# Performance work log

Hardware: AMD Instinct MI355X
Metric: run time of the kernel (lower is better)

The kernel has to match this reference:

```python
import jax, jax.numpy as jnp
import numpy as np

B, S, T = 64, 80, 20          # batch, video_len, caption_len
F, H, E, V, CD = 4096, 256, 256, 32000, 64  # feat, hidden, embed, vocab, coverage_dim
LN_EPS = 1e-5


def setup_inputs() -> dict:
    key = jax.random.key(0)
    ks = iter(jax.random.split(key, 40))
    rn = lambda *shape: jax.random.normal(next(ks), shape, dtype=jnp.float32) * 0.05
    inp = {
        "video_features": jax.random.normal(next(ks), (B, S, F), dtype=jnp.float32),
        "captions": jax.random.randint(next(ks), (B, T), 0, V),
        # video projection
        "W_vp": rn(H, F), "b_vp": jnp.zeros((H,), jnp.float32),
        # encoder LSTM (2 layers)
        "enc_Wih0": rn(4 * H, H), "enc_Whh0": rn(4 * H, H),
        "enc_bih0": jnp.zeros((4 * H,), jnp.float32), "enc_bhh0": jnp.zeros((4 * H,), jnp.float32),
        "enc_Wih1": rn(4 * H, H), "enc_Whh1": rn(4 * H, H),
        "enc_bih1": jnp.zeros((4 * H,), jnp.float32), "enc_bhh1": jnp.zeros((4 * H,), jnp.float32),
        # word embedding
        "emb": jax.random.uniform(next(ks), (V, E), jnp.float32, -0.1, 0.1),
        # decoder LSTM (input = E + H)
        "dec_Wih0": rn(4 * H, E + H), "dec_Whh0": rn(4 * H, H),
        "dec_bih0": jnp.zeros((4 * H,), jnp.float32), "dec_bhh0": jnp.zeros((4 * H,), jnp.float32),
        "dec_Wih1": rn(4 * H, H), "dec_Whh1": rn(4 * H, H),
        "dec_bih1": jnp.zeros((4 * H,), jnp.float32), "dec_bhh1": jnp.zeros((4 * H,), jnp.float32),
        # attention
        "att_Wh": rn(H, H), "att_Ws": rn(H, H),
        "att_v": jax.random.normal(next(ks), (H,), dtype=jnp.float32) * 0.1,
        "att_Wc": rn(H, CD),
        "cov_w": rn(CD, 1, 3), "cov_b": jnp.zeros((CD,), jnp.float32),
        # output layernorm + projection
        "ln_g": jnp.ones((H,), jnp.float32), "ln_b": jnp.zeros((H,), jnp.float32),
        "W_out": rn(V, H), "b_out": jnp.zeros((V,), jnp.float32),
    }
    return inp


def _lstm_cell(x, h, c, Wih, Whh, bih, bhh):
    z = x @ Wih.T + h @ Whh.T + bih + bhh
    i, f, g, o = jnp.split(z, 4, axis=-1)  # torch gate order: i, f, g, o
    c_new = jax.nn.sigmoid(f) * c + jax.nn.sigmoid(i) * jnp.tanh(g)
    h_new = jax.nn.sigmoid(o) * jnp.tanh(c_new)
    return h_new, c_new


def reference(video_features, captions, W_vp, b_vp,
              enc_Wih0, enc_Whh0, enc_bih0, enc_bhh0,
              enc_Wih1, enc_Whh1, enc_bih1, enc_bhh1,
              emb,
              dec_Wih0, dec_Whh0, dec_bih0, dec_bhh0,
              dec_Wih1, dec_Whh1, dec_bih1, dec_bhh1,
              att_Wh, att_Ws, att_v, att_Wc, cov_w, cov_b,
              ln_g, ln_b, W_out, b_out):
    b = video_features.shape[0]
    # ---- encoder ----
    vp = video_features @ W_vp.T + b_vp  # [B,S,H]

    def enc_step(carry, x_t):
        h1, c1, h2, c2 = carry
        h1, c1 = _lstm_cell(x_t, h1, c1, enc_Wih0, enc_Whh0, enc_bih0, enc_bhh0)
        h2, c2 = _lstm_cell(h1, h2, c2, enc_Wih1, enc_Whh1, enc_bih1, enc_bhh1)
        return (h1, c1, h2, c2), h2

    z = jnp.zeros((b, H), vp.dtype)
    (eh1, ec1, eh2, ec2), enc_out = jax.lax.scan(enc_step, (z, z, z, z), vp.transpose(1, 0, 2))
    enc_out = enc_out.transpose(1, 0, 2)  # [B,S,H]

    enc_proj = enc_out @ att_Wh.T  # [B,S,H], invariant over decode steps
    cov_k = cov_w[:, 0, :]          # [CD,3]

    def dec_step(carry, tok):
        h1, c1, h2, c2, cov = carry
        # attention with coverage (decoder_hidden[0][-1] == top-layer h)
        padded = jnp.pad(cov, ((0, 0), (1, 1)))
        win = jnp.stack([padded[:, :-2], padded[:, 1:-1], padded[:, 2:]], axis=-1)  # [B,S,3]
        cov_feat = jnp.einsum("bsk,ck->bsc", win, cov_k) + cov_b  # conv1d k=3 pad=1
        cov_proj = cov_feat @ att_Wc.T                              # [B,S,H]
        dec_proj = h2 @ att_Ws.T                                    # [B,H]
        energy = jnp.tanh(enc_proj + dec_proj[:, None, :] + cov_proj)
        scores = energy @ att_v                                     # [B,S]
        attn = jax.nn.softmax(scores, axis=1)
        ctx = jnp.einsum("bs,bsh->bh", attn, enc_out)
        new_cov = cov + attn
        # decoder LSTM step
        x = jnp.concatenate([emb[tok], ctx], axis=-1)  # [B,E+H]
        h1, c1 = _lstm_cell(x, h1, c1, dec_Wih0, dec_Whh0, dec_bih0, dec_bhh0)
        h2, c2 = _lstm_cell(h1, h2, c2, dec_Wih1, dec_Whh1, dec_bih1, dec_bhh1)
        # layernorm + vocab projection
        mu = jnp.mean(h2, axis=-1, keepdims=True)
        var = jnp.mean((h2 - mu) ** 2, axis=-1, keepdims=True)
        normed = (h2 - mu) * jax.lax.rsqrt(var + LN_EPS) * ln_g + ln_b
        logits = normed @ W_out.T + b_out  # [B,V]
        return (h1, c1, h2, c2, new_cov), logits

    cov0 = jnp.zeros((b, enc_out.shape[1]), enc_out.dtype)
    _, logits = jax.lax.scan(dec_step, (eh1, ec1, eh2, ec2, cov0), captions.T)
    return logits.transpose(1, 0, 2)  # [B,T,V]
```

## Files before the change

kernel.cpp:

```cpp
#include <hip/hip_runtime.h>
#include <math.h>

#define BB 64
#define SS 80
#define TT 20
#define FF 4096
#define HH 256
#define VV 32000

typedef __attribute__((ext_vector_type(8))) short bf16x8;
typedef __attribute__((ext_vector_type(4))) float f32x4;

__device__ __forceinline__ float fsig(float x){ return 1.f/(1.f+__expf(-x)); }
__device__ __forceinline__ float ftanh(float x){
    float xc = fminf(fmaxf(x,-15.f),15.f);
    float e = __expf(2.f*xc);
    return (e-1.f)/(e+1.f);
}
__device__ __forceinline__ unsigned int f2b(float x){
    unsigned int u = __float_as_uint(x);
    return (u + 0x7fffu + ((u>>16)&1u)) >> 16;
}
__device__ __forceinline__ float b2f(unsigned short u){
    return __uint_as_float(((unsigned)u)<<16);
}
__device__ __forceinline__ float dot2bf(unsigned w, unsigned hp, float acc){
    float r;
    asm("v_dot2_f32_bf16 %0, %1, %2, %3" : "=v"(r) : "v"(w), "v"(hp), "v"(acc));
    return r;
}
__device__ __forceinline__ void pack8(const float* __restrict__ s, unsigned short* __restrict__ d){
    float4 a = *reinterpret_cast<const float4*>(s);
    float4 b = *reinterpret_cast<const float4*>(s+4);
    uint4 o;
    o.x = f2b(a.x) | (f2b(a.y)<<16);
    o.y = f2b(a.z) | (f2b(a.w)<<16);
    o.z = f2b(b.x) | (f2b(b.y)<<16);
    o.w = f2b(b.z) | (f2b(b.w)<<16);
    *reinterpret_cast<uint4*>(d) = o;
}

__global__ __launch_bounds__(256) void prep_kernel(
    const float* __restrict__ eWhh0, const float* __restrict__ eWih1, const float* __restrict__ eWhh1,
    const float* __restrict__ dWih0, const float* __restrict__ dWhh0, const float* __restrict__ dWih1,
    const float* __restrict__ dWhh1, const float* __restrict__ attWs, const float* __restrict__ attWc,
    const float* __restrict__ cov_w, const float* __restrict__ cov_b,
    const float* __restrict__ e_bih0, const float* __restrict__ e_bhh0,
    const float* __restrict__ e_bih1, const float* __restrict__ e_bhh1,
    const float* __restrict__ d_bih0, const float* __restrict__ d_bhh0,
    const float* __restrict__ d_bih1, const float* __restrict__ d_bhh1,
    const float* __restrict__ W_out, const float* __restrict__ attWh,
    const float* __restrict__ W_vp,  const float* __restrict__ eWih0,
    const float* __restrict__ video, const float* __restrict__ emb,
    const int*   __restrict__ captions,
    unsigned* pkWhh0e, unsigned* pkWhh1e, unsigned* pkWih1e,
    unsigned* pkWx0d, unsigned* pkWhh0d, unsigned* pkWih1d, unsigned* pkWhh1d,
    unsigned* pkWs,
    float* M3, float* attcb,
    float* b0e, float* b1e, float* b0d, float* b1d,
    unsigned short* Wob, unsigned short* Whb,
    unsigned short* Wvpb, unsigned short* Wih0b, unsigned short* dWx0b,
    unsigned short* embg, unsigned short* vidb)
{
    int blk = blockIdx.x, tid = threadIdx.x;
    if (blk < 1856){
        const float* src; int stride, coff, Nj, j0, k0; unsigned* dst;
        if (blk < 1792){
            int mat = blk >> 8, tl = blk & 255;
            switch(mat){
                case 0: src=eWhh0; stride=256; coff=0;   dst=pkWhh0e; break;
                case 1: src=eWhh1; stride=256; coff=0;   dst=pkWhh1e; break;
                case 2: src=eWih1; stride=256; coff=0;   dst=pkWih1e; break;
                case 3: src=dWih0; stride=512; coff=256; dst=pkWx0d;  break;
                case 4: src=dWhh0; stride=256; coff=0;   dst=pkWhh0d; break;
                case 5: src=dWih1; stride=256; coff=0;   dst=pkWih1d; break;
                default:src=dWhh1; stride=256; coff=0;   dst=pkWhh1d; break;
            }
            Nj = 1024; j0 = (tl>>3)*32; k0 = (tl&7)*32;
        } else {
            int tl = blk - 1792;
            src=attWs; stride=256; coff=0; dst=pkWs;
            Nj = 256; j0 = (tl>>3)*32; k0 = (tl&7)*32;
        }
        __shared__ float t1[32][33];
        int r = tid >> 5, c = tid & 31;
        #pragma unroll
        for (int i=0;i<4;i++)
            t1[r+i*8][c] = src[(size_t)(j0+r+i*8)*stride + coff + k0 + c];
        __syncthreads();
        int k2l = tid >> 5, j = tid & 31;
        #pragma unroll
        for (int i=0;i<2;i++){
            int kq = k2l + i*8;
            dst[(size_t)(k0/2 + kq)*Nj + j0 + j] =
                f2b(t1[j][2*kq]) | (f2b(t1[j][2*kq+1])<<16);
        }
        return;
    }
    if (blk == 1856){
        float m0=0.f,m1=0.f,m2=0.f,cb=0.f;
        for (int c=0;c<64;c++){
            float w = attWc[tid*64+c];
            m0 += w*cov_w[c*3+0]; m1 += w*cov_w[c*3+1]; m2 += w*cov_w[c*3+2];
            cb += w*cov_b[c];
        }
        M3[tid*3+0]=m0; M3[tid*3+1]=m1; M3[tid*3+2]=m2; attcb[tid]=cb;
        return;
    }
    if (blk == 1857){
        for (int i=tid;i<1024;i+=256){
            b0e[i]=e_bih0[i]+e_bhh0[i]; b1e[i]=e_bih1[i]+e_bhh1[i];
            b0d[i]=d_bih0[i]+d_bhh0[i]; b1d[i]=d_bih1[i]+d_bhh1[i];
        }
        return;
    }
    if (blk >= 6818){ size_t i=(size_t)(blk-6818)*2048 + tid*8; pack8(video+i, vidb+i); return; }
    if (blk >= 6658){ size_t i=(size_t)(blk-6658)*2048 + tid*8;
        int row = (int)(i>>8), col = (int)(i&255);
        pack8(emb + (size_t)captions[row]*256 + col, embg+i); return; }
    if (blk >= 6530){ size_t i=(size_t)(blk-6530)*2048 + tid*8;
        int j = (int)(i>>8), k = (int)(i&255);
        pack8(dWih0 + (size_t)j*512 + k, dWx0b+i); return; }
    if (blk >= 6402){ size_t i=(size_t)(blk-6402)*2048 + tid*8; pack8(eWih0+i, Wih0b+i); return; }
    if (blk >= 5890){ size_t i=(size_t)(blk-5890)*2048 + tid*8; pack8(W_vp+i, Wvpb+i); return; }
    if (blk >= 5858){ size_t i=(size_t)(blk-5858)*2048 + tid*8; pack8(attWh+i, Whb+i); return; }
    { size_t i=(size_t)(blk-1858)*2048 + tid*8; pack8(W_out+i, Wob+i); }
}

template<bool OUTBF>
__global__ __launch_bounds__(256) void gemm_bf16(int K, int N,
    const short* __restrict__ A, const short* __restrict__ Bw,
    const float* __restrict__ bias, void* __restrict__ out)
{
    int w = threadIdx.x >> 6, lane = threadIdx.x & 63;
    int m0 = blockIdx.y*64 + w*16, n0 = blockIdx.x*64;
    int row = lane & 15, kg = lane >> 4;
    const short* arow = A + (size_t)(m0 + row)*K + kg*8;
    f32x4 acc[4] = {};
    for (int kk=0; kk<K; kk+=32){
        bf16x8 a = *reinterpret_cast<const bf16x8*>(arow + kk);
        #pragma unroll
        for (int f=0; f<4; ++f){
            bf16x8 bfr = *reinterpret_cast<const bf16x8*>(
                Bw + (size_t)(n0 + f*16 + row)*K + kk + kg*8);
            acc[f] = __builtin_amdgcn_mfma_f32_16x16x32_bf16(a, bfr, acc[f], 0, 0, 0);
        }
    }
    #pragma unroll
    for (int f=0; f<4; ++f){
        int n = n0 + f*16 + row;
        float bv = bias ? bias[n] : 0.f;
        #pragma unroll
        for (int r=0; r<4; ++r){
            int m = m0 + kg*4 + r;
            float v = acc[f][r] + bv;
            if (OUTBF) ((unsigned short*)out)[(size_t)m*N + n] = (unsigned short)f2b(v);
            else       ((float*)out)[(size_t)m*N + n] = v;
        }
    }
}

#define RES_DOTS(a0,a1,a2,a3)                                              \
    _Pragma("unroll")                                                      \
    for (int g=0; g<24; g++){                                              \
        uint4 hc = hp4[g];                                                 \
        a0=dot2bf(wv0[4*g+0],hc.x,a0); a1=dot2bf(wv1[4*g+0],hc.x,a1);      \
        a2=dot2bf(wv0[4*g+1],hc.y,a2); a3=dot2bf(wv1[4*g+1],hc.y,a3);      \
        a0=dot2bf(wv0[4*g+2],hc.z,a0); a1=dot2bf(wv1[4*g+2],hc.z,a1);      \
        a2=dot2bf(wv0[4*g+3],hc.w,a2); a3=dot2bf(wv1[4*g+3],hc.w,a3);      \
    }                                                                      \
    _Pragma("unroll")                                                      \
    for (int g=0; g<8; g++){                                               \
        uint4 hc = hp4[24+g];                                              \
        uint4 w0 = ws[j0][g ^ p0];                                         \
        uint4 w1 = ws[j1][g ^ p1];                                         \
        a0=dot2bf(w0.x,hc.x,a0); a1=dot2bf(w1.x,hc.x,a1);                  \
        a2=dot2bf(w0.y,hc.y,a2); a3=dot2bf(w1.y,hc.y,a3);                  \
        a0=dot2bf(w0.z,hc.z,a0); a1=dot2bf(w1.z,hc.z,a1);                  \
        a2=dot2bf(w0.w,hc.w,a2); a3=dot2bf(w1.w,hc.w,a3);                  \
    }

__global__ __launch_bounds__(512, 2) void enc_pipe(
    const float* __restrict__ zx0,
    const unsigned* __restrict__ pkWhh0, const unsigned* __restrict__ pkWih1,
    const unsigned* __restrict__ pkWhh1, const float* __restrict__ b1e,
    unsigned* __restrict__ h1pub,
    float* __restrict__ z1pub,
    unsigned short* __restrict__ h2seq,
    unsigned short* __restrict__ hfin, float* __restrict__ cfin,
    unsigned* __restrict__ flagA, unsigned* __restrict__ flagB)
{
    __shared__ uint4 ws[1024][8];
    __shared__ uint4 hp4[32];
    __shared__ float zsf[256], zso[256];
    __shared__ float zsx[1024];
    int gid = blockIdx.x, tid = threadIdx.x;
    int stage = gid >> 6, b = gid & 63;
    const unsigned* pk = (stage==0) ? pkWhh0 : ((stage==1) ? pkWih1 : pkWhh1);
    int j0 = tid, j1 = tid + 512;
    unsigned wv0[96], wv1[96];
    #pragma unroll
    for (int kk=0; kk<96; kk++){
        wv0[kk] = pk[(size_t)kk*1024 + j0];
        wv1[kk] = pk[(size_t)kk*1024 + j1];
    }
    unsigned* wsu = (unsigned*)ws;
    for (int i = tid; i < 32*1024; i += 512){
        int kk = i >> 10, j = i & 1023;
        wsu[j*32 + (((kk>>2) ^ (j&7))<<2) + (kk&3)] = pk[(size_t)(96+kk)*1024 + j];
    }
    int p0 = j0 & 7, p1 = j1 & 7;

    if (stage == 0){
        float c = 0.f;
        if (tid < 128) ((unsigned*)hp4)[tid] = 0;
        __syncthreads();
        for (int t=0; t<SS; ++t){
            size_t row = (size_t)b*SS + t;
            float zxv0=0.f, zxv1=0.f, zxv2=0.f, zxv3=0.f;
            if (tid < 256){
                const float* zr = zx0 + row*1024;
                zxv0=zr[tid]; zxv1=zr[tid+256]; zxv2=zr[tid+512]; zxv3=zr[tid+768];
            }
            float a0=0.f,a1=0.f,a2=0.f,a3=0.f;
            RES_DOTS(a0,a1,a2,a3)
            if (tid >= 256){ zsf[tid-256] = a0+a2; zso[tid-256] = a1+a3; }
            __syncthreads();
            if (tid < 256){
                float i_ = zxv0 + a0+a2;
                float f_ = zxv1 + zsf[tid];
                float g_ = zxv2 + a1+a3;
                float o_ = zxv3 + zso[tid];
                float cn = fsig(f_)*c + fsig(i_)*ftanh(g_);
                c = cn;
                ((unsigned short*)hp4)[tid] = (unsigned short)f2b(fsig(o_)*ftanh(cn));
            }
            __syncthreads();
            if (tid < 128)
                __hip_atomic_store(&h1pub[row*128 + tid], ((unsigned*)hp4)[tid],
                                   __ATOMIC_RELAXED, __HIP_MEMORY_SCOPE_AGENT);
            asm volatile("s_waitcnt vmcnt(0)" ::: "memory");
            __syncthreads();
            if (tid == 0)
                __hip_atomic_store(&flagA[b], (unsigned)(t+1),
                                   __ATOMIC_RELAXED, __HIP_MEMORY_SCOPE_AGENT);
        }
        if (tid < 256){
            hfin[b*512 + tid] = ((unsigned short*)hp4)[tid];
            cfin[b*512 + tid] = c;
        }
    } else if (stage == 1){
        float bj0 = b1e[j0], bj1 = b1e[j1];
        __syncthreads();
        for (int t=0; t<SS; ++t){
            size_t row = (size_t)b*SS + t;
            if (tid == 0){
                while (__hip_atomic_load(&flagA[b], __ATOMIC_RELAXED,
                                         __HIP_MEMORY_SCOPE_AGENT) < (unsigned)(t+1))
                    __builtin_amdgcn_s_sleep(2);
            }
            __syncthreads();
            if (tid < 128)
                ((unsigned*)hp4)[tid] = __hip_atomic_load(&h1pub[row*128 + tid],
                                          __ATOMIC_RELAXED, __HIP_MEMORY_SCOPE_AGENT);
            __syncthreads();
            float a0=0.f,a1=0.f,a2=0.f,a3=0.f;
            RES_DOTS(a0,a1,a2,a3)
            __hip_atomic_store(&z1pub[row*1024 + j0], a0+a2+bj0,
                               __ATOMIC_RELAXED, __HIP_MEMORY_SCOPE_AGENT);
            __hip_atomic_store(&z1pub[row*1024 + j1], a1+a3+bj1,
                               __ATOMIC_RELAXED, __HIP_MEMORY_SCOPE_AGENT);
            asm volatile("s_waitcnt vmcnt(0)" ::: "memory");
            __syncthreads();
            if (tid == 0)
                __hip_atomic_store(&flagB[b], (unsigned)(t+1),
                                   __ATOMIC_RELAXED, __HIP_MEMORY_SCOPE_AGENT);
        }
    } else {
        float c = 0.f;
        if (tid < 128) ((unsigned*)hp4)[tid] = 0;
        __syncthreads();
        for (int t=0; t<SS; ++t){
            size_t row = (size_t)b*SS + t;
            if (tid == 0){
                while (__hip_atomic_load(&flagB[b], __ATOMIC_RELAXED,
                                         __HIP_MEMORY_SCOPE_AGENT) < (unsigned)(t+1))
                    __builtin_amdgcn_s_sleep(2);
            }
            __syncthreads();
            zsx[j0] = __hip_atomic_load(&z1pub[row*1024 + j0],
                        __ATOMIC_RELAXED, __HIP_MEMORY_SCOPE_AGENT);
            zsx[j1] = __hip_atomic_load(&z1pub[row*1024 + j1],
                        __ATOMIC_RELAXED, __HIP_MEMORY_SCOPE_AGENT);
            float a0=0.f,a1=0.f,a2=0.f,a3=0.f;
            RES_DOTS(a0,a1,a2,a3)
            if (tid >= 256){ zsf[tid-256] = a0+a2; zso[tid-256] = a1+a3; }
            __syncthreads();
            if (tid < 256){
                float i_ = zsx[tid]     + a0+a2;
                float f_ = zsx[tid+256] + zsf[tid];
                float g_ = zsx[tid+512] + a1+a3;
                float o_ = zsx[tid+768] + zso[tid];
                float cn = fsig(f_)*c + fsig(i_)*ftanh(g_);
                c = cn;
                float hn = fsig(o_)*ftanh(cn);
                unsigned short hb = (unsigned short)f2b(hn);
                ((unsigned short*)hp4)[tid] = hb;
                h2seq[row*256 + tid] = hb;
            }
            __syncthreads();
        }
        if (tid < 256){
            hfin[b*512 + 256 + tid] = ((unsigned short*)hp4)[tid];
            cfin[b*512 + 256 + tid] = c;
        }
    }
}

template<int ITERS>
__device__ __forceinline__ void dot_phase(const unsigned* __restrict__ wbase,
    const unsigned* __restrict__ hu, int k2base, int jq, float* __restrict__ zrow)
{
    float a0=0.f,a1=0.f,a2=0.f,a3=0.f;
    const uint4* wp = (const uint4*)(wbase + (size_t)k2base*1024 + jq*4);
    #pragma unroll 8
    for (int kk=0; kk<ITERS; ++kk){
        uint4 w = wp[(size_t)kk*256];
        unsigned hp = hu[k2base+kk];
        a0=dot2bf(w.x,hp,a0); a1=dot2bf(w.y,hp,a1);
        a2=dot2bf(w.z,hp,a2); a3=dot2bf(w.w,hp,a3);
    }
    zrow[jq*4+0]=a0; zrow[jq*4+1]=a1; zrow[jq*4+2]=a2; zrow[jq*4+3]=a3;
}

__global__ __launch_bounds__(1024) void dec_scan(
    const float* __restrict__ embproj,
    const unsigned* __restrict__ wx0, const unsigned* __restrict__ whh0,
    const unsigned* __restrict__ wih1, const unsigned* __restrict__ whh1,
    const unsigned* __restrict__ pkWs,
    const float* __restrict__ b1d,
    const unsigned short* __restrict__ encp,
    const unsigned short* __restrict__ enco,
    const float* __restrict__ att_v, const float* __restrict__ M3,
    const float* __restrict__ attcb,
    const float* __restrict__ ln_g, const float* __restrict__ ln_b,
    const float* __restrict__ encfC, const unsigned short* __restrict__ encfH,
    unsigned short* __restrict__ normedb)
{
    int b = blockIdx.x, tid = threadIdx.x;
    __shared__ unsigned short encpL[SS*256];
    __shared__ unsigned short encoL[SS*256];
    __shared__ unsigned short h1b[256], h2b[256], ctxb[256];
    __shared__ float c1s[256], c2s[256];
    __shared__ float zb[4][1024];
    __shared__ float covs[82], scs[80], attns[80], dps[256];
    __shared__ float red[16];
    {
        const uint4* sp = (const uint4*)(encp + (size_t)b*SS*256);
        const uint4* so = (const uint4*)(enco + (size_t)b*SS*256);
        uint4* dp = (uint4*)encpL;
        uint4* dq = (uint4*)encoL;
        for (int i=tid; i<SS*256/8; i+=1024){ dp[i] = sp[i]; dq[i] = so[i]; }
    }
    int h = tid & 255;
    float bz0=0.f,bz1=0.f,bz2=0.f,bz3=0.f, gg=0.f, bb2=0.f;
    if (tid < 256){
        h1b[tid] = encfH[b*512 + tid];
        h2b[tid] = encfH[b*512 + 256 + tid];
        c1s[tid] = encfC[b*512 + tid];
        c2s[tid] = encfC[b*512 + 256 + tid];
        bz0=b1d[tid]; bz1=b1d[tid+256]; bz2=b1d[tid+512]; bz3=b1d[tid+768];
        gg=ln_g[tid]; bb2=ln_b[tid];
    }
    if (tid < 82) covs[tid] = 0.f;
    int wv = tid >> 6, lane = tid & 63;
    float va[4], m30[4], m31[4], m32[4];
    #pragma unroll
    for (int i=0;i<4;i++){
        int hh = lane + i*64;
        va[i]=att_v[hh]; m30[i]=M3[hh*3]; m31[i]=M3[hh*3+1]; m32[i]=M3[hh*3+2];
    }
    int q   = tid >> 8;
    int jq  = tid & 255;
    int m1  = tid >> 9;
    int ks1 = (tid >> 8) & 1;
    const unsigned* h1u = (const unsigned*)h1b;
    const unsigned* h2u = (const unsigned*)h2b;
    const unsigned* cxu = (const unsigned*)ctxb;
    __syncthreads();
    for (int t=0; t<TT; ++t){
        {
            float acc = 0.f;
            const unsigned* wp = pkWs + (size_t)(q*32)*256 + h;
            #pragma unroll 8
            for (int kk=0; kk<32; ++kk)
                acc = dot2bf(wp[(size_t)kk*256], h2u[q*32+kk], acc);
            zb[q][h] = acc;
        }
        __syncthreads();
        if (tid < 256) dps[tid] = attcb[tid] + zb[0][tid]+zb[1][tid]+zb[2][tid]+zb[3][tid];
        __syncthreads();
        for (int s = wv*5; s < wv*5+5; ++s){
            float c0=covs[s], c1v=covs[s+1], c2v=covs[s+2];
            float p = 0.f;
            #pragma unroll
            for (int i=0;i<4;i++){
                int hh = lane + i*64;
                float e = b2f(encpL[s*256+hh]) + dps[hh]
                        + m30[i]*c0 + m31[i]*c1v + m32[i]*c2v;
                p += va[i]*ftanh(e);
            }
            #pragma unroll
            for (int off=32;off;off>>=1) p += __shfl_down(p, off);
            if (lane == 0) scs[s] = p;
        }
        __syncthreads();
        if (tid < 64){
            float a = scs[tid];
            float bsc = (tid < 16) ? scs[tid+64] : -3.4e38f;
            float mx = fmaxf(a, bsc);
            #pragma unroll
            for (int off=32;off;off>>=1) mx = fmaxf(mx, __shfl_xor(mx, off));
            float ea = __expf(a - mx);
            float eb = (tid < 16) ? __expf(bsc - mx) : 0.f;
            float sum = ea + eb;
            #pragma unroll
            for (int off=32;off;off>>=1) sum += __shfl_xor(sum, off);
            float inv = 1.f/sum;
            attns[tid] = ea*inv;
            if (tid < 16) attns[tid+64] = eb*inv;
        }
        __syncthreads();
        if (tid < 80) covs[tid+1] += attns[tid];
        {
            float acc = 0.f;
            for (int s=q*20; s<q*20+20; ++s)
                acc += attns[s]*b2f(encoL[s*256 + h]);
            zb[q][h] = acc;
        }
        __syncthreads();
        if (tid < 256)
            ctxb[h] = (unsigned short)f2b(zb[0][h]+zb[1][h]+zb[2][h]+zb[3][h]);
        float ep0=0.f,ep1=0.f,ep2=0.f,ep3=0.f;
        if (tid < 256){
            const float* er = embproj + ((size_t)b*TT + t)*1024;
            ep0=er[h]; ep1=er[h+256]; ep2=er[h+512]; ep3=er[h+768];
        }
        __syncthreads();
        dot_phase<64>(m1 ? whh0 : wx0, m1 ? h1u : cxu, ks1*64, jq, &zb[m1*2+ks1][0]);
        __syncthreads();
        if (tid < 256){
            float i_ = ep0+zb[0][h]+zb[1][h]+zb[2][h]+zb[3][h];
            float f_ = ep1+zb[0][h+256]+zb[1][h+256]+zb[2][h+256]+zb[3][h+256];
            float g_ = ep2+zb[0][h+512]+zb[1][h+512]+zb[2][h+512]+zb[3][h+512];
            float o_ = ep3+zb[0][h+768]+zb[1][h+768]+zb[2][h+768]+zb[3][h+768];
            float cn = fsig(f_)*c1s[h] + fsig(i_)*ftanh(g_);
            c1s[h] = cn;
            h1b[h] = (unsigned short)f2b(fsig(o_)*ftanh(cn));
        }
        __syncthreads();
        dot_phase<64>(m1 ? whh1 : wih1, m1 ? h2u : h1u, ks1*64, jq, &zb[m1*2+ks1][0]);
        __syncthreads();
        float hn = 0.f;
        if (tid < 256){
            float i_ = bz0+zb[0][h]+zb[1][h]+zb[2][h]+zb[3][h];
            float f_ = bz1+zb[0][h+256]+zb[1][h+256]+zb[2][h+256]+zb[3][h+256];
            float g_ = bz2+zb[0][h+512]+zb[1][h+512]+zb[2][h+512]+zb[3][h+512];
            float o_ = bz3+zb[0][h+768]+zb[1][h+768]+zb[2][h+768]+zb[3][h+768];
            float cn = fsig(f_)*c2s[h] + fsig(i_)*ftanh(g_);
            c2s[h] = cn;
            hn = fsig(o_)*ftanh(cn);
            h2b[h] = (unsigned short)f2b(hn);
        }
        float s1 = hn;
        #pragma unroll
        for (int off=32;off;off>>=1) s1 += __shfl_xor(s1, off);
        if (lane == 0) red[wv] = s1;
        __syncthreads();
        float mean = (red[0]+red[1]+red[2]+red[3]) * (1.f/256.f);
        __syncthreads();
        float d = (tid < 256) ? (hn - mean) : 0.f;
        float s2 = d*d;
        #pragma unroll
        for (int off=32;off;off>>=1) s2 += __shfl_xor(s2, off);
        if (lane == 0) red[wv] = s2;
        __syncthreads();
        float var = (red[0]+red[1]+red[2]+red[3]) * (1.f/256.f);
        if (tid < 256)
            normedb[((size_t)b*TT + t)*256 + h] =
                (unsigned short)f2b(d*rsqrtf(var + 1e-5f)*gg + bb2);
        __syncthreads();
    }
}

__global__ __launch_bounds__(256) void logits_mfma(
    const short* __restrict__ A, const short* __restrict__ Bw,
    const float* __restrict__ bias, float* __restrict__ out)
{
    int w = threadIdx.x >> 6, lane = threadIdx.x & 63;
    int n0 = blockIdx.x*64 + w*16;
    int row = lane & 15, kg = lane >> 4;
    bf16x8 bfr[8];
    const short* brow = Bw + (size_t)(n0 + row)*256 + kg*8;
    #pragma unroll
    for (int kk=0;kk<8;kk++) bfr[kk] = *reinterpret_cast<const bf16x8*>(brow + kk*32);
    float bv = bias[n0 + row];
    for (int mt=0; mt<80; ++mt){
        int m0 = mt*16;
        const short* arow = A + (size_t)(m0 + row)*256 + kg*8;
        f32x4 acc = {};
        #pragma unroll
        for (int kk=0;kk<8;kk++){
            bf16x8 a = *reinterpret_cast<const bf16x8*>(arow + kk*32);
            acc = __builtin_amdgcn_mfma_f32_16x16x32_bf16(a, bfr[kk], acc, 0, 0, 0);
        }
        #pragma unroll
        for (int r=0;r<4;r++){
            int m = m0 + kg*4 + r;
            out[(size_t)m*VV + n0 + row] = acc[r] + bv;
        }
    }
}

extern "C" void kernel_launch(void* const* d_in, const int* in_sizes, int n_in,
                              void* d_out, int out_size, void* d_ws, size_t ws_size,
                              hipStream_t stream)
{
    const float* video  = (const float*)d_in[0];
    const int*   caps   = (const int*)  d_in[1];
    const float* W_vp   = (const float*)d_in[2];
    const float* b_vp   = (const float*)d_in[3];
    const float* eWih0  = (const float*)d_in[4];
    const float* eWhh0  = (const float*)d_in[5];
    const float* e_bih0 = (const float*)d_in[6];
    const float* e_bhh0 = (const float*)d_in[7];
    const float* eWih1  = (const float*)d_in[8];
    const float* eWhh1  = (const float*)d_in[9];
    const float* e_bih1 = (const float*)d_in[10];
    const float* e_bhh1 = (const float*)d_in[11];
    const float* emb    = (const float*)d_in[12];
    const float* dWih0  = (const float*)d_in[13];
    const float* dWhh0  = (const float*)d_in[14];
    const float* d_bih0 = (const float*)d_in[15];
    const float* d_bhh0 = (const float*)d_in[16];
    const float* dWih1  = (const float*)d_in[17];
    const float* dWhh1  = (const float*)d_in[18];
    const float* d_bih1 = (const float*)d_in[19];
    const float* d_bhh1 = (const float*)d_in[20];
    const float* attWh  = (const float*)d_in[21];
    const float* attWs  = (const float*)d_in[22];
    const float* att_v  = (const float*)d_in[23];
    const float* attWc  = (const float*)d_in[24];
    const float* cov_w  = (const float*)d_in[25];
    const float* cov_b  = (const float*)d_in[26];
    const float* ln_g   = (const float*)d_in[27];
    const float* ln_b   = (const float*)d_in[28];
    const float* W_out  = (const float*)d_in[29];
    const float* b_out  = (const float*)d_in[30];
    float* out = (float*)d_out;

    float* W = (float*)d_ws;
    size_t o = 0;
    auto alloc = [&](size_t n){ size_t r = o; o += ((n + 63)/64)*64; return r; };

    float* U = W + alloc((size_t)10485760);
    unsigned short* vidb = (unsigned short*)U;
    float* z1pub = U;
    float* zx0     = W + alloc((size_t)SS*BB*1024);
    float* embproj = W + alloc((size_t)TT*BB*1024);
    unsigned short* vp_b  = (unsigned short*)(W + alloc((size_t)SS*BB*HH/2));
    unsigned short* embg  = (unsigned short*)(W + alloc((size_t)TT*BB*HH/2));
    unsigned short* encpb = (unsigned short*)(W + alloc((size_t)BB*SS*HH/2));
    unsigned short* normedb = (unsigned short*)(W + alloc((size_t)BB*TT*HH/2));
    unsigned* h1pub = (unsigned*)(W + alloc((size_t)SS*BB*128));
    unsigned short* h2seq = (unsigned short*)(W + alloc((size_t)SS*BB*HH/2));
    float* encfC   = W + alloc(BB*512);
    unsigned short* encfH = (unsigned short*)(W + alloc(BB*256));
    unsigned* flags = (unsigned*)(W + alloc(128));
    unsigned* pkWhh0e = (unsigned*)(W + alloc(128*1024));
    unsigned* pkWhh1e = (unsigned*)(W + alloc(128*1024));
    unsigned* pkWih1e = (unsigned*)(W + alloc(128*1024));
    unsigned* pkWx0d  = (unsigned*)(W + alloc(128*1024));
    unsigned* pkWhh0d = (unsigned*)(W + alloc(128*1024));
    unsigned* pkWih1d = (unsigned*)(W + alloc(128*1024));
    unsigned* pkWhh1d = (unsigned*)(W + alloc(128*1024));
    unsigned* pkWs    = (unsigned*)(W + alloc(128*256));
    float* M3      = W + alloc(768);
    float* attcb   = W + alloc(256);
    float* b0e     = W + alloc(1024);
    float* b1e     = W + alloc(1024);
    float* b0d     = W + alloc(1024);
    float* b1d     = W + alloc(1024);
    unsigned short* Wob   = (unsigned short*)(W + alloc((size_t)VV*HH/2));
    unsigned short* Whb   = (unsigned short*)(W + alloc(256*HH/2));
    unsigned short* Wvpb  = (unsigned short*)(W + alloc((size_t)HH*FF/2));
    unsigned short* Wih0b = (unsigned short*)(W + alloc(1024*HH/2));
    unsigned short* dWx0b = (unsigned short*)(W + alloc(1024*HH/2));
    (void)ws_size; (void)n_in; (void)in_sizes; (void)out_size;

    hipMemsetAsync(flags, 0, 128*sizeof(unsigned), stream);

    prep_kernel<<<17058, 256, 0, stream>>>(
        eWhh0, eWih1, eWhh1, dWih0, dWhh0, dWih1, dWhh1, attWs, attWc,
        cov_w, cov_b, e_bih0, e_bhh0, e_bih1, e_bhh1, d_bih0, d_bhh0, d_bih1, d_bhh1,
        W_out, attWh, W_vp, eWih0, video, emb, caps,
        pkWhh0e, pkWhh1e, pkWih1e, pkWx0d, pkWhh0d, pkWih1d, pkWhh1d, pkWs,
        M3, attcb, b0e, b1e, b0d, b1d,
        Wob, Whb, Wvpb, Wih0b, dWx0b, embg, vidb);

    gemm_bf16<true><<<dim3(4, 80), 256, 0, stream>>>(
        FF, HH, (const short*)vidb, (const short*)Wvpb, b_vp, vp_b);

    gemm_bf16<false><<<dim3(16, 80), 256, 0, stream>>>(
        HH, 1024, (const short*)vp_b, (const short*)Wih0b, b0e, zx0);

    gemm_bf16<false><<<dim3(16, 20), 256, 0, stream>>>(
        HH, 1024, (const short*)embg, (const short*)dWx0b, b0d, embproj);

    enc_pipe<<<192, 512, 0, stream>>>(zx0, pkWhh0e, pkWih1e, pkWhh1e, b1e,
                                      h1pub, z1pub, h2seq, encfH, encfC,
                                      flags, flags + 64);

    gemm_bf16<true><<<dim3(4, 80), 256, 0, stream>>>(
        HH, HH, (const short*)h2seq, (const short*)Whb, nullptr, encpb);

    dec_scan<<<64, 1024, 0, stream>>>(embproj, pkWx0d, pkWhh0d, pkWih1d, pkWhh1d,
                                      pkWs, b1d, encpb, h2seq, att_v, M3, attcb,
                                      ln_g, ln_b, encfC, encfH, normedb);

    logits_mfma<<<VV/64, 256, 0, stream>>>(
        (const short*)normedb, (const short*)Wob, b_out, out);
}
```

Before: 1.100 ms.

## Split decoder scan into attention blocks and MFMA LSTM gate blocks with flag sync

Replaces the per-batch decoder scan kernel (64 blocks of 1024 threads, dot2 GEMVs) with a fused kernel of 72 blocks. 64 blocks do per-batch attention and layernorm. 8 extra blocks compute the decoder LSTM gates for the whole batch with bf16 MFMA, each block owning a slice of the hidden dimension. Context and hidden states pass between blocks through global buffers guarded by atomic flags and spin waits. The aim is to replace the latency-bound per-batch GEMVs with batched matrix-core work. The cost is cross-block synchronisation latency on every timestep, and all 72 blocks must be co-resident or the spin waits deadlock.

```diff
diff --git a/kernel.cpp b/kernel.cpp
--- a/kernel.cpp
+++ b/kernel.cpp
@@ -38,6 +38,19 @@
     o.z = f2b(b.x) | (f2b(b.y)<<16);
     o.w = f2b(b.z) | (f2b(b.w)<<16);
     *reinterpret_cast<uint4*>(d) = o;
+}
+__device__ __forceinline__ unsigned aload(const unsigned* p){
+    return __hip_atomic_load((unsigned*)p, __ATOMIC_RELAXED, __HIP_MEMORY_SCOPE_AGENT);
+}
+__device__ __forceinline__ void astore(unsigned* p, unsigned v){
+    __hip_atomic_store(p, v, __ATOMIC_RELAXED, __HIP_MEMORY_SCOPE_AGENT);
+}
+__device__ __forceinline__ void waitF(const unsigned* f, int mask, unsigned tgt, int lane){
+    for (;;){
+        unsigned v = aload(&f[lane & mask]);
+        if (__all(v >= tgt)) break;
+        __builtin_amdgcn_s_sleep(1);
+    }
 }
 
 __global__ __launch_bounds__(256) void prep_kernel(
@@ -53,40 +66,33 @@
     const float* __restrict__ W_vp,  const float* __restrict__ eWih0,
     const float* __restrict__ video, const float* __restrict__ emb,
     const int*   __restrict__ captions,
-    unsigned* pkWhh0e, unsigned* pkWhh1e, unsigned* pkWih1e,
-    unsigned* pkWx0d, unsigned* pkWhh0d, unsigned* pkWih1d, unsigned* pkWhh1d,
-    unsigned* pkWs,
+    unsigned* pkWhh0e, unsigned* pkWih1e, unsigned* pkWhh1e, unsigned* pkWs,
     float* M3, float* attcb,
     float* b0e, float* b1e, float* b0d, float* b1d,
     unsigned short* Wob, unsigned short* Whb,
     unsigned short* Wvpb, unsigned short* Wih0b, unsigned short* dWx0b,
-    unsigned short* embg, unsigned short* vidb)
+    unsigned short* embg,
+    unsigned short* Wx0p, unsigned short* Whh0p, unsigned short* Wih1p, unsigned short* Whh1p,
+    unsigned short* vidb)
 {
     int blk = blockIdx.x, tid = threadIdx.x;
-    if (blk < 1856){
-        const float* src; int stride, coff, Nj, j0, k0; unsigned* dst;
-        if (blk < 1792){
+    if (blk < 832){
+        const float* src; int Nj, j0, k0; unsigned* dst;
+        if (blk < 768){
             int mat = blk >> 8, tl = blk & 255;
-            switch(mat){
-                case 0: src=eWhh0; stride=256; coff=0;   dst=pkWhh0e; break;
-                case 1: src=eWhh1; stride=256; coff=0;   dst=pkWhh1e; break;
-                case 2: src=eWih1; stride=256; coff=0;   dst=pkWih1e; break;
-                case 3: src=dWih0; stride=512; coff=256; dst=pkWx0d;  break;
-                case 4: src=dWhh0; stride=256; coff=0;   dst=pkWhh0d; break;
-                case 5: src=dWih1; stride=256; coff=0;   dst=pkWih1d; break;
-                default:src=dWhh1; stride=256; coff=0;   dst=pkWhh1d; break;
-            }
+            src = (mat==0) ? eWhh0 : ((mat==1) ? eWih1 : eWhh1);
+            dst = (mat==0) ? pkWhh0e : ((mat==1) ? pkWih1e : pkWhh1e);
             Nj = 1024; j0 = (tl>>3)*32; k0 = (tl&7)*32;
         } else {
-            int tl = blk - 1792;
-            src=attWs; stride=256; coff=0; dst=pkWs;
+            int tl = blk - 768;
+            src=attWs; dst=pkWs;
             Nj = 256; j0 = (tl>>3)*32; k0 = (tl&7)*32;
         }
         __shared__ float t1[32][33];
         int r = tid >> 5, c = tid & 31;
         #pragma unroll
         for (int i=0;i<4;i++)
-            t1[r+i*8][c] = src[(size_t)(j0+r+i*8)*stride + coff + k0 + c];
+            t1[r+i*8][c] = src[(size_t)(j0+r+i*8)*256 + k0 + c];
         __syncthreads();
         int k2l = tid >> 5, j = tid & 31;
         #pragma unroll
@@ -97,7 +103,7 @@
         }
         return;
     }
-    if (blk == 1856){
+    if (blk == 832){
         float m0=0.f,m1=0.f,m2=0.f,cb=0.f;
         for (int c=0;c<64;c++){
             float w = attWc[tid*64+c];
@@ -107,24 +113,30 @@
         M3[tid*3+0]=m0; M3[tid*3+1]=m1; M3[tid*3+2]=m2; attcb[tid]=cb;
         return;
     }
-    if (blk == 1857){
+    if (blk == 833){
         for (int i=tid;i<1024;i+=256){
             b0e[i]=e_bih0[i]+e_bhh0[i]; b1e[i]=e_bih1[i]+e_bhh1[i];
             b0d[i]=d_bih0[i]+d_bhh0[i]; b1d[i]=d_bih1[i]+d_bhh1[i];
         }
         return;
     }
-    if (blk >= 6818){ size_t i=(size_t)(blk-6818)*2048 + tid*8; pack8(video+i, vidb+i); return; }
-    if (blk >= 6658){ size_t i=(size_t)(blk-6658)*2048 + tid*8;
+    if (blk >= 6306){ size_t i=(size_t)(blk-6306)*2048 + tid*8; pack8(video+i, vidb+i); return; }
+    if (blk >= 6178){ size_t i=(size_t)(blk-6178)*2048 + tid*8; pack8(dWhh1+i, Whh1p+i); return; }
+    if (blk >= 6050){ size_t i=(size_t)(blk-6050)*2048 + tid*8; pack8(dWih1+i, Wih1p+i); return; }
+    if (blk >= 5922){ size_t i=(size_t)(blk-5922)*2048 + tid*8; pack8(dWhh0+i, Whh0p+i); return; }
+    if (blk >= 5794){ size_t i=(size_t)(blk-5794)*2048 + tid*8;
+        int j = (int)(i>>8), k = (int)(i&255);
+        pack8(dWih0 + (size_t)j*512 + 256 + k, Wx0p+i); return; }
+    if (blk >= 5634){ size_t i=(size_t)(blk-5634)*2048 + tid*8;
         int row = (int)(i>>8), col = (int)(i&255);
         pack8(emb + (size_t)captions[row]*256 + col, embg+i); return; }
-    if (blk >= 6530){ size_t i=(size_t)(blk-6530)*2048 + tid*8;
+    if (blk >= 5506){ size_t i=(size_t)(blk-5506)*2048 + tid*8;
         int j = (int)(i>>8), k = (int)(i&255);
         pack8(dWih0 + (size_t)j*512 + k, dWx0b+i); return; }
-    if (blk >= 6402){ size_t i=(size_t)(blk-6402)*2048 + tid*8; pack8(eWih0+i, Wih0b+i); return; }
-    if (blk >= 5890){ size_t i=(size_t)(blk-5890)*2048 + tid*8; pack8(W_vp+i, Wvpb+i); return; }
-    if (blk >= 5858){ size_t i=(size_t)(blk-5858)*2048 + tid*8; pack8(attWh+i, Whb+i); return; }
-    { size_t i=(size_t)(blk-1858)*2048 + tid*8; pack8(W_out+i, Wob+i); }
+    if (blk >= 5378){ size_t i=(size_t)(blk-5378)*2048 + tid*8; pack8(eWih0+i, Wih0b+i); return; }
+    if (blk >= 4866){ size_t i=(size_t)(blk-4866)*2048 + tid*8; pack8(W_vp+i, Wvpb+i); return; }
+    if (blk >= 4834){ size_t i=(size_t)(blk-4834)*2048 + tid*8; pack8(attWh+i, Whb+i); return; }
+    { size_t i=(size_t)(blk-834)*2048 + tid*8; pack8(W_out+i, Wob+i); }
 }
 
 template<bool OUTBF>
@@ -184,8 +196,7 @@
     const float* __restrict__ zx0,
     const unsigned* __restrict__ pkWhh0, const unsigned* __restrict__ pkWih1,
     const unsigned* __restrict__ pkWhh1, const float* __restrict__ b1e,
-    unsigned* __restrict__ h1pub,
-    float* __restrict__ z1pub,
+    unsigned* __restrict__ h1pub, float* __restrict__ z1pub,
     unsigned short* __restrict__ h2seq,
     unsigned short* __restrict__ hfin, float* __restrict__ cfin,
     unsigned* __restrict__ flagA, unsigned* __restrict__ flagB)
@@ -236,14 +247,10 @@
                 ((unsigned short*)hp4)[tid] = (unsigned short)f2b(fsig(o_)*ftanh(cn));
             }
             __syncthreads();
-            if (tid < 128)
-                __hip_atomic_store(&h1pub[row*128 + tid], ((unsigned*)hp4)[tid],
-                                   __ATOMIC_RELAXED, __HIP_MEMORY_SCOPE_AGENT);
+            if (tid < 128) astore(&h1pub[row*128 + tid], ((unsigned*)hp4)[tid]);
             asm volatile("s_waitcnt vmcnt(0)" ::: "memory");
             __syncthreads();
-            if (tid == 0)
-                __hip_atomic_store(&flagA[b], (unsigned)(t+1),
-                                   __ATOMIC_RELAXED, __HIP_MEMORY_SCOPE_AGENT);
+            if (tid == 0) astore(&flagA[b], (unsigned)(t+1));
         }
         if (tid < 256){
             hfin[b*512 + tid] = ((unsigned short*)hp4)[tid];
@@ -255,26 +262,18 @@
         for (int t=0; t<SS; ++t){
             size_t row = (size_t)b*SS + t;
             if (tid == 0){
-                while (__hip_atomic_load(&flagA[b], __ATOMIC_RELAXED,
-                                         __HIP_MEMORY_SCOPE_AGENT) < (unsigned)(t+1))
-                    __builtin_amdgcn_s_sleep(2);
-            }
-            __syncthreads();
-            if (tid < 128)
-                ((unsigned*)hp4)[tid] = __hip_atomic_load(&h1pub[row*128 + tid],
-                                          __ATOMIC_RELAXED, __HIP_MEMORY_SCOPE_AGENT);
+                while (aload(&flagA[b]) < (unsigned)(t+1)) __builtin_amdgcn_s_sleep(2);
+            }
+            __syncthreads();
+            if (tid < 128) ((unsigned*)hp4)[tid] = aload(&h1pub[row*128 + tid]);
             __syncthreads();
             float a0=0.f,a1=0.f,a2=0.f,a3=0.f;
             RES_DOTS(a0,a1,a2,a3)
-            __hip_atomic_store(&z1pub[row*1024 + j0], a0+a2+bj0,
-                               __ATOMIC_RELAXED, __HIP_MEMORY_SCOPE_AGENT);
-            __hip_atomic_store(&z1pub[row*1024 + j1], a1+a3+bj1,
-                               __ATOMIC_RELAXED, __HIP_MEMORY_SCOPE_AGENT);
+            astore((unsigned*)&z1pub[row*1024 + j0], __float_as_uint(a0+a2+bj0));
+            astore((unsigned*)&z1pub[row*1024 + j1], __float_as_uint(a1+a3+bj1));
             asm volatile("s_waitcnt vmcnt(0)" ::: "memory");
             __syncthreads();
-            if (tid == 0)
-                __hip_atomic_store(&flagB[b], (unsigned)(t+1),
-                                   __ATOMIC_RELAXED, __HIP_MEMORY_SCOPE_AGENT);
+            if (tid == 0) astore(&flagB[b], (unsigned)(t+1));
         }
     } else {
         float c = 0.f;
@@ -283,15 +282,11 @@
         for (int t=0; t<SS; ++t){
             size_t row = (size_t)b*SS + t;
             if (tid == 0){
-                while (__hip_atomic_load(&flagB[b], __ATOMIC_RELAXED,
-                                         __HIP_MEMORY_SCOPE_AGENT) < (unsigned)(t+1))
-                    __builtin_amdgcn_s_sleep(2);
-            }
-            __syncthreads();
-            zsx[j0] = __hip_atomic_load(&z1pub[row*1024 + j0],
-                        __ATOMIC_RELAXED, __HIP_MEMORY_SCOPE_AGENT);
-            zsx[j1] = __hip_atomic_load(&z1pub[row*1024 + j1],
-                        __ATOMIC_RELAXED, __HIP_MEMORY_SCOPE_AGENT);
+                while (aload(&flagB[b]) < (unsigned)(t+1)) __builtin_amdgcn_s_sleep(2);
+            }
+            __syncthreads();
+            zsx[j0] = __uint_as_float(aload((unsigned*)&z1pub[row*1024 + j0]));
+            zsx[j1] = __uint_as_float(aload((unsigned*)&z1pub[row*1024 + j1]));
             float a0=0.f,a1=0.f,a2=0.f,a3=0.f;
             RES_DOTS(a0,a1,a2,a3)
             if (tid >= 256){ zsf[tid-256] = a0+a2; zso[tid-256] = a1+a3; }
@@ -317,179 +312,278 @@
     }
 }
 
-template<int ITERS>
-__device__ __forceinline__ void dot_phase(const unsigned* __restrict__ wbase,
-    const unsigned* __restrict__ hu, int k2base, int jq, float* __restrict__ zrow)
-{
-    float a0=0.f,a1=0.f,a2=0.f,a3=0.f;
-    const uint4* wp = (const uint4*)(wbase + (size_t)k2base*1024 + jq*4);
-    #pragma unroll 8
-    for (int kk=0; kk<ITERS; ++kk){
-        uint4 w = wp[(size_t)kk*256];
-        unsigned hp = hu[k2base+kk];
-        a0=dot2bf(w.x,hp,a0); a1=dot2bf(w.y,hp,a1);
-        a2=dot2bf(w.z,hp,a2); a3=dot2bf(w.w,hp,a3);
-    }
-    zrow[jq*4+0]=a0; zrow[jq*4+1]=a1; zrow[jq*4+2]=a2; zrow[jq*4+3]=a3;
-}
-
-__global__ __launch_bounds__(1024) void dec_scan(
+__global__ __launch_bounds__(512, 2) void dec_fused(
     const float* __restrict__ embproj,
-    const unsigned* __restrict__ wx0, const unsigned* __restrict__ whh0,
-    const unsigned* __restrict__ wih1, const unsigned* __restrict__ whh1,
+    const unsigned short* __restrict__ Wx0p, const unsigned short* __restrict__ Whh0p,
+    const unsigned short* __restrict__ Wih1p, const unsigned short* __restrict__ Whh1p,
     const unsigned* __restrict__ pkWs,
     const float* __restrict__ b1d,
-    const unsigned short* __restrict__ encp,
-    const unsigned short* __restrict__ enco,
+    const unsigned short* __restrict__ encp, const unsigned short* __restrict__ enco,
     const float* __restrict__ att_v, const float* __restrict__ M3,
     const float* __restrict__ attcb,
     const float* __restrict__ ln_g, const float* __restrict__ ln_b,
     const float* __restrict__ encfC, const unsigned short* __restrict__ encfH,
+    unsigned* __restrict__ ctxpub, unsigned* __restrict__ h1pub, unsigned* __restrict__ h2pub,
+    unsigned* __restrict__ hInitF, unsigned* __restrict__ ctxF,
+    unsigned* __restrict__ h1F, unsigned* __restrict__ h2F,
     unsigned short* __restrict__ normedb)
 {
-    int b = blockIdx.x, tid = threadIdx.x;
-    __shared__ unsigned short encpL[SS*256];
-    __shared__ unsigned short encoL[SS*256];
-    __shared__ unsigned short h1b[256], h2b[256], ctxb[256];
-    __shared__ float c1s[256], c2s[256];
-    __shared__ float zb[4][1024];
-    __shared__ float covs[82], scs[80], attns[80], dps[256];
-    __shared__ float red[16];
-    {
-        const uint4* sp = (const uint4*)(encp + (size_t)b*SS*256);
-        const uint4* so = (const uint4*)(enco + (size_t)b*SS*256);
-        uint4* dp = (uint4*)encpL;
-        uint4* dq = (uint4*)encoL;
-        for (int i=tid; i<SS*256/8; i+=1024){ dp[i] = sp[i]; dq[i] = so[i]; }
-    }
-    int h = tid & 255;
-    float bz0=0.f,bz1=0.f,bz2=0.f,bz3=0.f, gg=0.f, bb2=0.f;
-    if (tid < 256){
-        h1b[tid] = encfH[b*512 + tid];
-        h2b[tid] = encfH[b*512 + 256 + tid];
-        c1s[tid] = encfC[b*512 + tid];
-        c2s[tid] = encfC[b*512 + 256 + tid];
-        bz0=b1d[tid]; bz1=b1d[tid+256]; bz2=b1d[tid+512]; bz3=b1d[tid+768];
-        gg=ln_g[tid]; bb2=ln_b[tid];
-    }
-    if (tid < 82) covs[tid] = 0.f;
-    int wv = tid >> 6, lane = tid & 63;
-    float va[4], m30[4], m31[4], m32[4];
-    #pragma unroll
-    for (int i=0;i<4;i++){
-        int hh = lane + i*64;
-        va[i]=att_v[hh]; m30[i]=M3[hh*3]; m31[i]=M3[hh*3+1]; m32[i]=M3[hh*3+2];
-    }
-    int q   = tid >> 8;
-    int jq  = tid & 255;
-    int m1  = tid >> 9;
-    int ks1 = (tid >> 8) & 1;
-    const unsigned* h1u = (const unsigned*)h1b;
-    const unsigned* h2u = (const unsigned*)h2b;
-    const unsigned* cxu = (const unsigned*)ctxb;
-    __syncthreads();
-    for (int t=0; t<TT; ++t){
+    __shared__ float smem[37280];
+    int blk = blockIdx.x, tid = threadIdx.x, lane = tid & 63;
+
+    if (blk < 64){
+        int b = blk;
+        unsigned short* encpL = (unsigned short*)smem;
+        unsigned short* encoL = (unsigned short*)(smem+10240);
+        unsigned short* h2b   = (unsigned short*)(smem+20480);
+        unsigned short* ctxb  = (unsigned short*)(smem+20608);
+        float* zb0  = smem+20736;
+        float* zb1  = smem+21760;
+        float* covs = smem+22784;
+        float* scs  = smem+22872;
+        float* attns= smem+22956;
+        float* dps  = smem+23040;
+        float* red  = smem+23296;
         {
-            float acc = 0.f;
-            const unsigned* wp = pkWs + (size_t)(q*32)*256 + h;
-            #pragma unroll 8
-            for (int kk=0; kk<32; ++kk)
-                acc = dot2bf(wp[(size_t)kk*256], h2u[q*32+kk], acc);
-            zb[q][h] = acc;
-        }
+            const uint4* sp = (const uint4*)(encp + (size_t)b*SS*256);
+            const uint4* so = (const uint4*)(enco + (size_t)b*SS*256);
+            uint4* dp = (uint4*)encpL;
+            uint4* dq = (uint4*)encoL;
+            for (int i=tid; i<SS*256/8; i+=512){ dp[i] = sp[i]; dq[i] = so[i]; }
+        }
+        if (tid < 128){
+            ((unsigned*)h2b)[tid] = ((const unsigned*)(encfH + (size_t)b*512 + 256))[tid];
+            astore(&h1pub[b*128 + tid], ((const unsigned*)(encfH + (size_t)b*512))[tid]);
+            astore(&h2pub[b*128 + tid], ((const unsigned*)(encfH + (size_t)b*512 + 256))[tid]);
+        }
+        if (tid < 82) covs[tid] = 0.f;
+        float gg=0.f, bb2=0.f;
+        if (tid < 256){ gg = ln_g[tid]; bb2 = ln_b[tid]; }
+        int wv = tid >> 6;
+        float va[4], m30[4], m31[4], m32[4];
+        #pragma unroll
+        for (int i=0;i<4;i++){
+            int hh = lane + i*64;
+            va[i]=att_v[hh]; m30[i]=M3[hh*3]; m31[i]=M3[hh*3+1]; m32[i]=M3[hh*3+2];
+        }
+        asm volatile("s_waitcnt vmcnt(0)" ::: "memory");
         __syncthreads();
-        if (tid < 256) dps[tid] = attcb[tid] + zb[0][tid]+zb[1][tid]+zb[2][tid]+zb[3][tid];
+        if (tid == 0) astore(&hInitF[b], 1u);
+        const unsigned* h2u = (const unsigned*)h2b;
+        int q = tid >> 8, h = tid & 255;
+        for (int t=0; t<TT; ++t){
+            {
+                float acc = q ? 0.f : attcb[h];
+                const unsigned* wp = pkWs + (size_t)(q*64)*256 + h;
+                #pragma unroll 8
+                for (int kk=0; kk<64; ++kk)
+                    acc = dot2bf(wp[(size_t)kk*256], h2u[q*64+kk], acc);
+                (q ? zb1 : zb0)[h] = acc;
+            }
+            __syncthreads();
+            if (tid < 256) dps[tid] = zb0[tid] + zb1[tid];
+            __syncthreads();
+            for (int s = wv*10; s < wv*10+10; ++s){
+                float c0=covs[s], c1v=covs[s+1], c2v=covs[s+2];
+                float p = 0.f;
+                #pragma unroll
+                for (int i=0;i<4;i++){
+                    int hh = lane + i*64;
+                    float e = b2f(encpL[s*256+hh]) + dps[hh]
+                            + m30[i]*c0 + m31[i]*c1v + m32[i]*c2v;
+                    p += va[i]*ftanh(e);
+                }
+                #pragma unroll
+                for (int off=32;off;off>>=1) p += __shfl_down(p, off);
+                if (lane == 0) scs[s] = p;
+            }
+            __syncthreads();
+            if (tid < 64){
+                float a = scs[tid];
+                float bsc = (tid < 16) ? scs[tid+64] : -3.4e38f;
+                float mx = fmaxf(a, bsc);
+                #pragma unroll
+                for (int off=32;off;off>>=1) mx = fmaxf(mx, __shfl_xor(mx, off));
+                float ea = __expf(a - mx);
+                float eb = (tid < 16) ? __expf(bsc - mx) : 0.f;
+                float sum = ea + eb;
+                #pragma unroll
+                for (int off=32;off;off>>=1) sum += __shfl_xor(sum, off);
+                float inv = 1.f/sum;
+                attns[tid] = ea*inv;
+                if (tid < 16) attns[tid+64] = eb*inv;
+            }
+            __syncthreads();
+            if (tid < 80) covs[tid+1] += attns[tid];
+            {
+                float acc = 0.f;
+                for (int s=q*40; s<q*40+40; ++s)
+                    acc += attns[s]*b2f(encoL[s*256 + h]);
+                (q ? zb1 : zb0)[h] = acc;
+            }
+            __syncthreads();
+            if (tid < 256) ctxb[h] = (unsigned short)f2b(zb0[h] + zb1[h]);
+            __syncthreads();
+            if (tid < 128) astore(&ctxpub[b*128 + tid], ((unsigned*)ctxb)[tid]);
+            asm volatile("s_waitcnt vmcnt(0)" ::: "memory");
+            __syncthreads();
+            if (tid == 0) astore(&ctxF[b], (unsigned)(t+1));
+            waitF(h2F, 7, (unsigned)(t+1), lane);
+            if (tid < 128) ((unsigned*)h2b)[tid] = aload(&h2pub[b*128 + tid]);
+            __syncthreads();
+            float hn = (tid < 256) ? b2f(h2b[tid]) : 0.f;
+            float s1 = hn;
+            #pragma unroll
+            for (int off=32;off;off>>=1) s1 += __shfl_xor(s1, off);
+            if (tid < 256 && lane == 0) red[wv] = s1;
+            __syncthreads();
+            float mean = (red[0]+red[1]+red[2]+red[3]) * (1.f/256.f);
+            __syncthreads();
+            float d = (tid < 256) ? (hn - mean) : 0.f;
+            float s2 = d*d;
+            #pragma unroll
+            for (int off=32;off;off>>=1) s2 += __shfl_xor(s2, off);
+            if (tid < 256 && lane == 0) red[wv] = s2;
+            __syncthreads();
+            float var = (red[0]+red[1]+red[2]+red[3]) * (1.f/256.f);
+            if (tid < 256)
+                normedb[((size_t)b*TT + t)*256 + h] =
+                    (unsigned short)f2b(d*rsqrtf(var + 1e-5f)*gg + bb2);
+            __syncthreads();
+        }
+    } else {
+        int g = blk - 64;
+        unsigned* XA = (unsigned*)smem;
+        unsigned* XB = XA + 8192;
+        unsigned* XC = XB + 8192;
+        float* zbuf = (float*)(XC + 8192);
+        float* c1   = zbuf + 8448;
+        float* c2   = c1 + 2048;
+        float* b1dL = c2 + 2048;
+        int wvv = tid >> 6, kg = lane >> 4, l15 = lane & 15;
+        int j_l = wvv*16 + l15;
+        int gate = j_l >> 5, hh_l = j_l & 31;
+        int jglob = gate*256 + g*32 + hh_l;
+        bf16x8 wx0f[8], wh0f[8], wi1f[8], wh1f[8];
+        #pragma unroll
+        for (int ks=0; ks<8; ++ks){
+            wx0f[ks] = *(const bf16x8*)(Wx0p  + (size_t)jglob*256 + ks*32 + kg*8);
+            wh0f[ks] = *(const bf16x8*)(Whh0p + (size_t)jglob*256 + ks*32 + kg*8);
+            wi1f[ks] = *(const bf16x8*)(Wih1p + (size_t)jglob*256 + ks*32 + kg*8);
+            wh1f[ks] = *(const bf16x8*)(Whh1p + (size_t)jglob*256 + ks*32 + kg*8);
+        }
+        for (int i = tid; i < 2048; i += 512){
+            int bb = i >> 5, hh = i & 31;
+            c1[hh*64 + bb] = encfC[bb*512 + g*32 + hh];
+            c2[hh*64 + bb] = encfC[bb*512 + 256 + g*32 + hh];
+        }
+        if (tid < 128) b1dL[tid] = b1d[(tid>>5)*256 + g*32 + (tid&31)];
+        waitF(hInitF, 63, 1u, lane);
+        for (int i = tid; i < 8192; i += 512){
+            XB[i] = aload(&h1pub[i]);
+            XC[i] = aload(&h2pub[i]);
+        }
+        asm volatile("s_waitcnt vmcnt(0)" ::: "memory");
         __syncthreads();
-        for (int s = wv*5; s < wv*5+5; ++s){
-            float c0=covs[s], c1v=covs[s+1], c2v=covs[s+2];
-            float p = 0.f;
+        int pwb = tid >> 3, pwh4 = (tid & 7)*4;
+        for (int t=0; t<TT; ++t){
+            f32x4 acc0[4] = {}; f32x4 acc1[4] = {};
             #pragma unroll
-            for (int i=0;i<4;i++){
-                int hh = lane + i*64;
-                float e = b2f(encpL[s*256+hh]) + dps[hh]
-                        + m30[i]*c0 + m31[i]*c1v + m32[i]*c2v;
-                p += va[i]*ftanh(e);
-            }
+            for (int ks=0; ks<8; ++ks){
+                #pragma unroll
+                for (int bt=0; bt<4; ++bt){
+                    bf16x8 xf = *(const bf16x8*)(XB + (bt*16 + l15)*128 + ks*16 + kg*4);
+                    acc0[bt] = __builtin_amdgcn_mfma_f32_16x16x32_bf16(wh0f[ks], xf, acc0[bt], 0,0,0);
+                    bf16x8 yf = *(const bf16x8*)(XC + (bt*16 + l15)*128 + ks*16 + kg*4);
+                    acc1[bt] = __builtin_amdgcn_mfma_f32_16x16x32_bf16(wh1f[ks], yf, acc1[bt], 0,0,0);
+                }
+            }
+            waitF(ctxF, 63, (unsigned)(t+1), lane);
+            for (int i = tid; i < 8192; i += 512) XA[i] = aload(&ctxpub[i]);
+            asm volatile("s_waitcnt vmcnt(0)" ::: "memory");
+            __syncthreads();
             #pragma unroll
-            for (int off=32;off;off>>=1) p += __shfl_down(p, off);
-            if (lane == 0) scs[s] = p;
-        }
-        __syncthreads();
-        if (tid < 64){
-            float a = scs[tid];
-            float bsc = (tid < 16) ? scs[tid+64] : -3.4e38f;
-            float mx = fmaxf(a, bsc);
+            for (int ks=0; ks<8; ++ks){
+                #pragma unroll
+                for (int bt=0; bt<4; ++bt){
+                    bf16x8 xf = *(const bf16x8*)(XA + (bt*16 + l15)*128 + ks*16 + kg*4);
+                    acc0[bt] = __builtin_amdgcn_mfma_f32_16x16x32_bf16(wx0f[ks], xf, acc0[bt], 0,0,0);
+                }
+            }
             #pragma unroll
-            for (int off=32;off;off>>=1) mx = fmaxf(mx, __shfl_xor(mx, off));
-            float ea = __expf(a - mx);
-            float eb = (tid < 16) ? __expf(bsc - mx) : 0.f;
-            float sum = ea + eb;
+            for (int bt=0; bt<4; ++bt)
+                #pragma unroll
+                for (int r=0; r<4; ++r)
+                    zbuf[(wvv*16 + kg*4 + r)*66 + bt*16 + l15] = acc0[bt][r];
+            __syncthreads();
+            {
+                const float* erow = embproj + ((size_t)pwb*TT + t)*1024 + g*32;
+                unsigned dw0, dw1; float hv[4];
+                #pragma unroll
+                for (int qq=0; qq<4; ++qq){
+                    int hh = pwh4 + qq;
+                    float i_ = zbuf[(hh     )*66 + pwb] + erow[hh];
+                    float f_ = zbuf[(32+hh)*66 + pwb] + erow[256+hh];
+                    float g_ = zbuf[(64+hh)*66 + pwb] + erow[512+hh];
+                    float o_ = zbuf[(96+hh)*66 + pwb] + erow[768+hh];
+                    float cn = fsig(f_)*c1[hh*64+pwb] + fsig(i_)*ftanh(g_);
+                    c1[hh*64+pwb] = cn;
+                    hv[qq] = fsig(o_)*ftanh(cn);
+                }
+                dw0 = f2b(hv[0]) | (f2b(hv[1])<<16);
+                dw1 = f2b(hv[2]) | (f2b(hv[3])<<16);
+                astore(&h1pub[pwb*128 + g*16 + (tid&7)*2    ], dw0);
+                astore(&h1pub[pwb*128 + g*16 + (tid&7)*2 + 1], dw1);
+            }
+            asm volatile("s_waitcnt vmcnt(0)" ::: "memory");
+            __syncthreads();
+            if (tid == 0) astore(&h1F[g], (unsigned)(t+1));
+            waitF(h1F, 7, (unsigned)(t+1), lane);
+            for (int i = tid; i < 8192; i += 512) XB[i] = aload(&h1pub[i]);
+            asm volatile("s_waitcnt vmcnt(0)" ::: "memory");
+            __syncthreads();
             #pragma unroll
-            for (int off=32;off;off>>=1) sum += __shfl_xor(sum, off);
-            float inv = 1.f/sum;
-            attns[tid] = ea*inv;
-            if (tid < 16) attns[tid+64] = eb*inv;
-        }
-        __syncthreads();
-        if (tid < 80) covs[tid+1] += attns[tid];
-        {
-            float acc = 0.f;
-            for (int s=q*20; s<q*20+20; ++s)
-                acc += attns[s]*b2f(encoL[s*256 + h]);
-            zb[q][h] = acc;
-        }
-        __syncthreads();
-        if (tid < 256)
-            ctxb[h] = (unsigned short)f2b(zb[0][h]+zb[1][h]+zb[2][h]+zb[3][h]);
-        float ep0=0.f,ep1=0.f,ep2=0.f,ep3=0.f;
-        if (tid < 256){
-            const float* er = embproj + ((size_t)b*TT + t)*1024;
-            ep0=er[h]; ep1=er[h+256]; ep2=er[h+512]; ep3=er[h+768];
-        }
-        __syncthreads();
-        dot_phase<64>(m1 ? whh0 : wx0, m1 ? h1u : cxu, ks1*64, jq, &zb[m1*2+ks1][0]);
-        __syncthreads();
-        if (tid < 256){
-            float i_ = ep0+zb[0][h]+zb[1][h]+zb[2][h]+zb[3][h];
-            float f_ = ep1+zb[0][h+256]+zb[1][h+256]+zb[2][h+256]+zb[3][h+256];
-            float g_ = ep2+zb[0][h+512]+zb[1][h+512]+zb[2][h+512]+zb[3][h+512];
-            float o_ = ep3+zb[0][h+768]+zb[1][h+768]+zb[2][h+768]+zb[3][h+768];
-            float cn = fsig(f_)*c1s[h] + fsig(i_)*ftanh(g_);
-            c1s[h] = cn;
-            h1b[h] = (unsigned short)f2b(fsig(o_)*ftanh(cn));
-        }
-        __syncthreads();
-        dot_phase<64>(m1 ? whh1 : wih1, m1 ? h2u : h1u, ks1*64, jq, &zb[m1*2+ks1][0]);
-        __syncthreads();
-        float hn = 0.f;
-        if (tid < 256){
-            float i_ = bz0+zb[0][h]+zb[1][h]+zb[2][h]+zb[3][h];
-            float f_ = bz1+zb[0][h+256]+zb[1][h+256]+zb[2][h+256]+zb[3][h+256];
-            float g_ = bz2+zb[0][h+512]+zb[1][h+512]+zb[2][h+512]+zb[3][h+512];
-            float o_ = bz3+zb[0][h+768]+zb[1][h+768]+zb[2][h+768]+zb[3][h+768];
-            float cn = fsig(f_)*c2s[h] + fsig(i_)*ftanh(g_);
-            c2s[h] = cn;
-            hn = fsig(o_)*ftanh(cn);
-            h2b[h] = (unsigned short)f2b(hn);
-        }
-        float s1 = hn;
-        #pragma unroll
-        for (int off=32;off;off>>=1) s1 += __shfl_xor(s1, off);
-        if (lane == 0) red[wv] = s1;
-        __syncthreads();
-        float mean = (red[0]+red[1]+red[2]+red[3]) * (1.f/256.f);
-        __syncthreads();
-        float d = (tid < 256) ? (hn - mean) : 0.f;
-        float s2 = d*d;
-        #pragma unroll
-        for (int off=32;off;off>>=1) s2 += __shfl_xor(s2, off);
-        if (lane == 0) red[wv] = s2;
-        __syncthreads();
-        float var = (red[0]+red[1]+red[2]+red[3]) * (1.f/256.f);
-        if (tid < 256)
-            normedb[((size_t)b*TT + t)*256 + h] =
-                (unsigned short)f2b(d*rsqrtf(var + 1e-5f)*gg + bb2);
-        __syncthreads();
+            for (int ks=0; ks<8; ++ks){
+                #pragma unroll
+                for (int bt=0; bt<4; ++bt){
+                    bf16x8 xf = *(const bf16x8*)(XB + (bt*16 + l15)*128 + ks*16 + kg*4);
+                    acc1[bt] = __builtin_amdgcn_mfma_f32_16x16x32_bf16(wi1f[ks], xf, acc1[bt], 0,0,0);
+                }
+            }
+            #pragma unroll
+            for (int bt=0; bt<4; ++bt)
+                #pragma unroll
+                for (int r=0; r<4; ++r)
+                    zbuf[(wvv*16 + kg*4 + r)*66 + bt*16 + l15] = acc1[bt][r];
+            __syncthreads();
+            {
+                unsigned dw0, dw1; float hv[4];
+                #pragma unroll
+                for (int qq=0; qq<4; ++qq){
+                    int hh = pwh4 + qq;
+                    float i_ = zbuf[(hh     )*66 + pwb] + b1dL[hh];
+                    float f_ = zbuf[(32+hh)*66 + pwb] + b1dL[32+hh];
+                    float g_ = zbuf[(64+hh)*66 + pwb] + b1dL[64+hh];
+                    float o_ = zbuf[(96+hh)*66 + pwb] + b1dL[96+hh];
+                    float cn = fsig(f_)*c2[hh*64+pwb] + fsig(i_)*ftanh(g_);
+                    c2[hh*64+pwb] = cn;
+                    hv[qq] = fsig(o_)*ftanh(cn);
+                }
+                dw0 = f2b(hv[0]) | (f2b(hv[1])<<16);
+                dw1 = f2b(hv[2]) | (f2b(hv[3])<<16);
+                astore(&h2pub[pwb*128 + g*16 + (tid&7)*2    ], dw0);
+                astore(&h2pub[pwb*128 + g*16 + (tid&7)*2 + 1], dw1);
+            }
+            asm volatile("s_waitcnt vmcnt(0)" ::: "memory");
+            __syncthreads();
+            if (tid == 0) astore(&h2F[g], (unsigned)(t+1));
+            if (t < TT-1){
+                waitF(h2F, 7, (unsigned)(t+1), lane);
+                for (int i = tid; i < 8192; i += 512) XC[i] = aload(&h2pub[i]);
+                asm volatile("s_waitcnt vmcnt(0)" ::: "memory");
+                __syncthreads();
+            }
+        }
     }
 }
 
@@ -572,19 +666,23 @@
     unsigned short* embg  = (unsigned short*)(W + alloc((size_t)TT*BB*HH/2));
     unsigned short* encpb = (unsigned short*)(W + alloc((size_t)BB*SS*HH/2));
     unsigned short* normedb = (unsigned short*)(W + alloc((size_t)BB*TT*HH/2));
-    unsigned* h1pub = (unsigned*)(W + alloc((size_t)SS*BB*128));
+    unsigned* h1pubE = (unsigned*)(W + alloc((size_t)SS*BB*128));
     unsigned short* h2seq = (unsigned short*)(W + alloc((size_t)SS*BB*HH/2));
     float* encfC   = W + alloc(BB*512);
     unsigned short* encfH = (unsigned short*)(W + alloc(BB*256));
-    unsigned* flags = (unsigned*)(W + alloc(128));
+    unsigned* eflags = (unsigned*)(W + alloc(128));
+    unsigned* dctx = (unsigned*)(W + alloc(8192));
+    unsigned* dh1  = (unsigned*)(W + alloc(8192));
+    unsigned* dh2  = (unsigned*)(W + alloc(8192));
+    unsigned* dflags = (unsigned*)(W + alloc(192));
     unsigned* pkWhh0e = (unsigned*)(W + alloc(128*1024));
+    unsigned* pkWih1e = (unsigned*)(W + alloc(128*1024));
     unsigned* pkWhh1e = (unsigned*)(W + alloc(128*1024));
-    unsigned* pkWih1e = (unsigned*)(W + alloc(128*1024));
-    unsigned* pkWx0d  = (unsigned*)(W + alloc(128*1024));
-    unsigned* pkWhh0d = (unsigned*)(W + alloc(128*1024));
-    unsigned* pkWih1d = (unsigned*)(W + alloc(128*1024));
-    unsigned* pkWhh1d = (unsigned*)(W + alloc(128*1024));
     unsigned* pkWs    = (unsigned*)(W + alloc(128*256));
+    unsigned short* Wx0p  = (unsigned short*)(W + alloc(1024*HH/2));
+    unsigned short* Whh0p = (unsigned short*)(W + alloc(1024*HH/2));
+    unsigned short* Wih1p = (unsigned short*)(W + alloc(1024*HH/2));
+    unsigned short* Whh1p = (unsigned short*)(W + alloc(1024*HH/2));
     float* M3      = W + alloc(768);
     float* attcb   = W + alloc(256);
     float* b0e     = W + alloc(1024);
@@ -598,15 +696,17 @@
     unsigned short* dWx0b = (unsigned short*)(W + alloc(1024*HH/2));
     (void)ws_size; (void)n_in; (void)in_sizes; (void)out_size;
 
-    hipMemsetAsync(flags, 0, 128*sizeof(unsigned), stream);
-
-    prep_kernel<<<17058, 256, 0, stream>>>(
+    hipMemsetAsync(eflags, 0, 128*sizeof(unsigned), stream);
+    hipMemsetAsync(dflags, 0, 192*sizeof(unsigned), stream);
+
+    prep_kernel<<<16546, 256, 0, stream>>>(
         eWhh0, eWih1, eWhh1, dWih0, dWhh0, dWih1, dWhh1, attWs, attWc,
         cov_w, cov_b, e_bih0, e_bhh0, e_bih1, e_bhh1, d_bih0, d_bhh0, d_bih1, d_bhh1,
         W_out, attWh, W_vp, eWih0, video, emb, caps,
-        pkWhh0e, pkWhh1e, pkWih1e, pkWx0d, pkWhh0d, pkWih1d, pkWhh1d, pkWs,
+        pkWhh0e, pkWih1e, pkWhh1e, pkWs,
         M3, attcb, b0e, b1e, b0d, b1d,
-        Wob, Whb, Wvpb, Wih0b, dWx0b, embg, vidb);
+        Wob, Whb, Wvpb, Wih0b, dWx0b, embg,
+        Wx0p, Whh0p, Wih1p, Whh1p, vidb);
 
     gemm_bf16<true><<<dim3(4, 80), 256, 0, stream>>>(
         FF, HH, (const short*)vidb, (const short*)Wvpb, b_vp, vp_b);
@@ -618,15 +718,18 @@
         HH, 1024, (const short*)embg, (const short*)dWx0b, b0d, embproj);
 
     enc_pipe<<<192, 512, 0, stream>>>(zx0, pkWhh0e, pkWih1e, pkWhh1e, b1e,
-                                      h1pub, z1pub, h2seq, encfH, encfC,
-                                      flags, flags + 64);
+                                      h1pubE, z1pub, h2seq, encfH, encfC,
+                                      eflags, eflags + 64);
 
     gemm_bf16<true><<<dim3(4, 80), 256, 0, stream>>>(
         HH, HH, (const short*)h2seq, (const short*)Whb, nullptr, encpb);
 
-    dec_scan<<<64, 1024, 0, stream>>>(embproj, pkWx0d, pkWhh0d, pkWih1d, pkWhh1d,
+    dec_fused<<<72, 512, 0, stream>>>(embproj, Wx0p, Whh0p, Wih1p, Whh1p,
                                       pkWs, b1d, encpb, h2seq, att_v, M3, attcb,
-                                      ln_g, ln_b, encfC, encfH, normedb);
+                                      ln_g, ln_b, encfC, encfH,
+                                      dctx, dh1, dh2,
+                                      dflags, dflags+64, dflags+128, dflags+136,
+                                      normedb);
 
     logits_mfma<<<VV/64, 256, 0, stream>>>(
         (const short*)normedb, (const short*)Wob, b_out, out);
```

Result: slower. 1.328 ms (+20.8%).
